# Optimization experiments

Measured on AMD Instinct MI355X. Metric: run time of the kernel, lower is better.

## Reference

```python
import jax, jax.numpy as jnp
import numpy as np

B, S, H, STATIC = 128, 128, 256, 2
BLOCKS = S // 2            # rotate_types = 2 for block_dim=2, allow_rot=True
DYN = 3 * BLOCKS           # dynamic channels: move / rotate_small / rotate_large


def setup_inputs() -> dict:
    key = jax.random.key(0)
    ks = jax.random.split(key, 16)
    p = lambda k, shape: (jax.random.normal(k, shape, jnp.float32) * 0.1)
    return {
        "static": jax.random.normal(ks[0], (B, STATIC + 1, S), jnp.float32),
        "dynamic": jnp.zeros((B, DYN, S), jnp.float32),
        "decoder_input": jax.random.normal(ks[1], (B, STATIC, 1), jnp.float32),
        # static/dynamic/decoder 1x1 conv encoders (weight [H, C_in], bias [H])
        "enc_s_W": p(ks[2], (H, STATIC)), "enc_s_b": p(ks[3], (H,)),
        "enc_d_W": p(ks[4], (H, DYN)),    "enc_d_b": p(ks[5], (H,)),
        "dec_W": p(ks[6], (H, STATIC)),   "dec_b": p(ks[7], (H,)),
        # single-layer GRU (torch layout: [3H, H] gates r,z,n)
        "gru_W_ih": p(ks[8], (3 * H, H)), "gru_W_hh": p(ks[9], (3 * H, H)),
        "gru_b_ih": p(ks[10], (3 * H,)),  "gru_b_hh": p(ks[11], (3 * H,)),
        # encoder attention and pointer heads: v [H], W [H, 3H]
        "attn_v": p(ks[12], (H,)), "attn_W": p(ks[13], (H, 3 * H)),
        "ptr_v": p(ks[14], (H,)),  "ptr_W": p(ks[15], (H, 3 * H)),
    }


def reference(static, dynamic, decoder_input,
              enc_s_W, enc_s_b, enc_d_W, enc_d_b, dec_W, dec_b,
              gru_W_ih, gru_W_hh, gru_b_ih, gru_b_hh,
              attn_v, attn_W, ptr_v, ptr_W):
    static_part = static[:, 1:, :]                                  # [B, STATIC, S]
    static_h = jnp.einsum('hi,bis->bhs', enc_s_W, static_part) + enc_s_b[None, :, None]
    dynamic_h = jnp.einsum('hi,bis->bhs', enc_d_W, dynamic) + enc_d_b[None, :, None]

    # initial mask from dynamic state (move + rotate feasibility)
    bn = dynamic.shape[1] // 3
    move = dynamic[:, :bn, :].sum(1)
    dyn_mask = dynamic[:, bn:2 * bn, :].sum(1) * dynamic[:, 2 * bn:3 * bn, :].sum(1) + move
    logmask = jnp.where(dyn_mask != 0, -jnp.inf, 0.0)               # log(current_mask), [B, S]

    hsz = gru_W_hh.shape[1]
    h0 = jnp.zeros((static.shape[0], hsz), static.dtype)            # GRU default zero state

    def gru_cell(x, h):
        gi = x @ gru_W_ih.T + gru_b_ih
        gh = h @ gru_W_hh.T + gru_b_hh
        ir, iz, inn = jnp.split(gi, 3, -1)
        hr, hz, hn = jnp.split(gh, 3, -1)
        r = jax.nn.sigmoid(ir + hr)
        z = jax.nn.sigmoid(iz + hz)
        n = jnp.tanh(inn + r * hn)
        return (1.0 - z) * n + z * h

    def step(carry, _):
        h_prev, dec_in = carry
        dec_h = jnp.einsum('hi,bi->bh', dec_W, dec_in[:, :, 0]) + dec_b   # decoder 1x1 conv
        h = gru_cell(dec_h, h_prev)                                       # rnn_out == new hidden
        rnn_b = jnp.broadcast_to(h[:, :, None], static_h.shape)
        hid = jnp.concatenate([static_h, dynamic_h, rnn_b], axis=1)       # [B, 3H, S]
        attn = jax.nn.softmax(
            jnp.einsum('h,bhs->bs', attn_v,
                       jnp.tanh(jnp.einsum('hk,bks->bhs', attn_W, hid))), axis=-1)
        context = jnp.einsum('bs,bhs->bh', attn, static_h)
        ctx_b = jnp.broadcast_to(context[:, :, None], static_h.shape)
        energy = jnp.concatenate([static_h, dynamic_h, ctx_b], axis=1)    # [B, 3H, S]
        logits = jnp.einsum('h,bhs->bs', ptr_v,
                            jnp.tanh(jnp.einsum('hk,bks->bhs', ptr_W, energy)))
        probs = jax.nn.softmax(logits + logmask, axis=-1)                 # [B, S]
        ptr = jnp.argmax(probs, axis=1)                                   # greedy (eval mode)
        logp = jnp.log(jnp.max(probs, axis=1))
        new_dec = jax.lax.stop_gradient(
            jnp.take_along_axis(static_part, ptr[:, None, None], axis=2))  # [B, STATIC, 1]
        return (h, new_dec), (ptr, logp)

    (_, _), (ptrs, logps) = jax.lax.scan(step, (h0, decoder_input), None,
                                         length=static_part.shape[2])
    tour_idx = ptrs.T    # [B, S]
    tour_logp = logps.T  # [B, S]
    return tour_idx, tour_logp
```

## Files before the change

kernel.cpp:

```cpp
#include <hip/hip_runtime.h>
#include <hip/hip_bf16.h>
#include <math.h>

#define BB   128
#define SS   128
#define HH   256
#define DYNN 192

#define OFF_FLAG  0
#define OFF_G     64
#define OFF_G0    (OFF_G + 1536)
#define OFF_M1A   (OFF_G0 + 768)
#define OFF_CA    (OFF_M1A + 512)
#define OFF_M1P   (OFF_CA + 256)
#define OFF_CP    (OFF_M1P + 512)
#define OFF_M3P   (OFF_CP + 256)
#define OFF_CP3   (OFF_M3P + 512)
#define OFF_LM    (OFF_CP3 + 256)
#define OFF_M2A   (OFF_LM + 16384)
#define OFF_M2P   (OFF_M2A + 49152)
#define OFF_BASEA (OFF_M2P + 49152)
#define OFF_BASEP (OFF_BASEA + 4194304)
#define OFF_END   (OFF_BASEP + 4194304)

__device__ __forceinline__ float tanh_fast(float x) {
    float e = __builtin_amdgcn_exp2f(x * 2.885390081777927f);
    return 1.0f - 2.0f * __builtin_amdgcn_rcpf(e + 1.0f);
}

__device__ __forceinline__ void ybar(int* cnt, bool arrive, int target) {
    if (arrive && (threadIdx.x & 63) == 0)
        __hip_atomic_fetch_add(cnt, 1, __ATOMIC_RELEASE, __HIP_MEMORY_SCOPE_WORKGROUP);
    while (__hip_atomic_load(cnt, __ATOMIC_ACQUIRE, __HIP_MEMORY_SCOPE_WORKGROUP) < target)
        __builtin_amdgcn_s_sleep(1);
}

__global__ void k1_logmask(const float* __restrict__ dyn, float* __restrict__ lm,
                           int* __restrict__ flag) {
    int g = blockIdx.x * 256 + threadIdx.x;
    if (g >= BB * SS) return;
    int b = g >> 7, s = g & 127;
    const float* p = dyn + (size_t)b * DYNN * SS + s;
    float mv = 0.f, m1 = 0.f, m2 = 0.f;
    bool nz = false;
    for (int i = 0; i < 64; ++i)        { float v = p[(size_t)i * SS]; mv += v; nz |= (v != 0.f); }
    for (int i = 64; i < 128; ++i)      { float v = p[(size_t)i * SS]; m1 += v; nz |= (v != 0.f); }
    for (int i = 128; i < 192; ++i)     { float v = p[(size_t)i * SS]; m2 += v; nz |= (v != 0.f); }
    float dm = m1 * m2 + mv;
    lm[g] = (dm != 0.f) ? -__builtin_inff() : 0.f;
    if (nz) atomicOr(flag, 1);
}

__global__ void k0a_folds(const float* __restrict__ Wih, const float* __restrict__ bih,
                          const float* __restrict__ dW,  const float* __restrict__ db,
                          const float* __restrict__ aW,  const float* __restrict__ pW,
                          const float* __restrict__ esW, const float* __restrict__ esb,
                          const float* __restrict__ edb, float* __restrict__ wsf) {
    int idx = blockIdx.x * 256 + threadIdx.x;
    float* G   = wsf + OFF_G;
    float* g0  = wsf + OFF_G0;
    float* M1a = wsf + OFF_M1A;
    float* ca  = wsf + OFF_CA;
    float* M1p = wsf + OFF_M1P;
    float* cp  = wsf + OFF_CP;
    float* M3p = wsf + OFF_M3P;
    float* cp3 = wsf + OFF_CP3;
    if (idx < 1536) {
        int r = idx >> 1, j = idx & 1;
        float a = 0.f;
        for (int k = 0; k < 256; ++k) a += Wih[r * 256 + k] * dW[k * 2 + j];
        G[idx] = a;
    } else if (idx < 2304) {
        int r = idx - 1536;
        float a = 0.f;
        for (int k = 0; k < 256; ++k) a += Wih[r * 256 + k] * db[k];
        g0[r] = a + bih[r];
    } else if (idx < 2816) {
        int t = idx - 2304; int h = t >> 1, j = t & 1;
        float a = 0.f;
        for (int k = 0; k < 256; ++k) a += aW[h * 768 + k] * esW[k * 2 + j];
        M1a[t] = a;
    } else if (idx < 3072) {
        int h = idx - 2816;
        float a = 0.f, b2 = 0.f;
        for (int k = 0; k < 256; ++k) a  += aW[h * 768 + k]       * esb[k];
        for (int k = 0; k < 256; ++k) b2 += aW[h * 768 + 256 + k] * edb[k];
        ca[h] = a + b2;
    } else if (idx < 3584) {
        int t = idx - 3072; int h = t >> 1, j = t & 1;
        float a = 0.f;
        for (int k = 0; k < 256; ++k) a += pW[h * 768 + k] * esW[k * 2 + j];
        M1p[t] = a;
    } else if (idx < 3840) {
        int h = idx - 3584;
        float a = 0.f, b2 = 0.f;
        for (int k = 0; k < 256; ++k) a  += pW[h * 768 + k]       * esb[k];
        for (int k = 0; k < 256; ++k) b2 += pW[h * 768 + 256 + k] * edb[k];
        cp[h] = a + b2;
    } else if (idx < 4352) {
        int t = idx - 3840; int h = t >> 1, j = t & 1;
        float a = 0.f;
        for (int k = 0; k < 256; ++k) a += pW[h * 768 + 512 + k] * esW[k * 2 + j];
        M3p[t] = a;
    } else if (idx < 4608) {
        int h = idx - 4352;
        float a = 0.f;
        for (int k = 0; k < 256; ++k) a += pW[h * 768 + 512 + k] * esb[k];
        cp3[h] = a;
    }
}

__global__ void k0b_m2(const float* __restrict__ aW, const float* __restrict__ pW,
                       const float* __restrict__ edW, float* __restrict__ wsf,
                       const int* __restrict__ flag) {
    if (*flag == 0) return;
    int idx = blockIdx.x * 256 + threadIdx.x;
    if (idx >= 2 * 49152) return;
    int which = idx / 49152;
    int t = idx % 49152;
    int h = t / DYNN, i = t % DYNN;
    const float* W = which ? pW : aW;
    float a = 0.f;
    for (int k = 0; k < 256; ++k) a += W[h * 768 + 256 + k] * edW[k * DYNN + i];
    wsf[(which ? OFF_M2P : OFF_M2A) + t] = a;
}

__global__ void k2_bases(const float* __restrict__ stat, const float* __restrict__ dyn,
                         float* __restrict__ wsf, const int* __restrict__ flag) {
    if (*flag == 0) return;
    __shared__ float col[DYNN];
    __shared__ float s01[2];
    const float* M1a = wsf + OFF_M1A; const float* ca  = wsf + OFF_CA;
    const float* M1p = wsf + OFF_M1P; const float* cp  = wsf + OFF_CP;
    const float* M2a = wsf + OFF_M2A; const float* M2p = wsf + OFF_M2P;
    float* basea = wsf + OFF_BASEA;   float* basep = wsf + OFF_BASEP;
    for (int pair = blockIdx.x; pair < BB * SS; pair += gridDim.x) {
        int b = pair >> 7, s = pair & 127;
        if (threadIdx.x < DYNN) col[threadIdx.x] = dyn[((size_t)b * DYNN + threadIdx.x) * SS + s];
        if (threadIdx.x == DYNN) {
            s01[0] = stat[((size_t)b * 3 + 1) * SS + s];
            s01[1] = stat[((size_t)b * 3 + 2) * SS + s];
        }
        __syncthreads();
        int h = threadIdx.x;
        float aa = fmaf(M1a[h * 2], s01[0], fmaf(M1a[h * 2 + 1], s01[1], ca[h]));
        float pp = fmaf(M1p[h * 2], s01[0], fmaf(M1p[h * 2 + 1], s01[1], cp[h]));
        for (int i = 0; i < DYNN; ++i) {
            aa = fmaf(M2a[h * DYNN + i], col[i], aa);
            pp = fmaf(M2p[h * DYNN + i], col[i], pp);
        }
        basea[((size_t)b * SS + s) * HH + h] = aa;
        basep[((size_t)b * SS + s) * HH + h] = pp;
        __syncthreads();
    }
}

__global__ __launch_bounds__(1024, 4) void k3_seq(
    const float* __restrict__ stat, const float* __restrict__ dec_inp,
    const float* __restrict__ Whh, const float* __restrict__ bhh_g,
    const float* __restrict__ aW, const float* __restrict__ av,
    const float* __restrict__ pv, const float* __restrict__ wsf,
    int allow_general, float* __restrict__ out) {
    const int b = blockIdx.x;
    const int tid = threadIdx.x;

    __shared__ float sh_gh[768], sh_hv[256], sh_t1[256], sh_a[128];
    __shared__ float sh_sp0[128], sh_sp1[128], sh_lm[128];
    __shared__ float sh_M1a[512], sh_M1p[512], sh_M3p[512];
    __shared__ float sh_ca[256], sh_cp[256], sh_cp3[256];
    __shared__ float sh_G[1536], sh_g0[768], sh_bhh[768];
    __shared__ float sh_va[256], sh_vp[256];
    __shared__ float sh_scal[4];
    __shared__ int ycnt;

    const float* G_   = wsf + OFF_G;   const float* g0_  = wsf + OFF_G0;
    const float* M1a_ = wsf + OFF_M1A; const float* ca_  = wsf + OFF_CA;
    const float* M1p_ = wsf + OFF_M1P; const float* cp_  = wsf + OFF_CP;
    const float* M3p_ = wsf + OFF_M3P; const float* cp3_ = wsf + OFF_CP3;
    const float* lm_  = wsf + OFF_LM;
    const float* basea = wsf + OFF_BASEA;
    const float* basep = wsf + OFF_BASEP;
    const int* flag = (const int*)wsf;

    for (int i = tid; i < 1536; i += 1024) sh_G[i] = G_[i];
    for (int i = tid; i < 768; i += 1024) {
        sh_g0[i] = g0_[i];
        float bv = bhh_g[i];
        sh_bhh[i] = bv;
        sh_gh[i] = bv;
    }
    for (int i = tid; i < 512; i += 1024) { sh_M1a[i] = M1a_[i]; sh_M1p[i] = M1p_[i]; sh_M3p[i] = M3p_[i]; }
    for (int i = tid; i < 256; i += 1024) {
        sh_ca[i] = ca_[i]; sh_cp[i] = cp_[i]; sh_cp3[i] = cp3_[i];
        sh_va[i] = av[i];  sh_vp[i] = pv[i];  sh_hv[i] = 0.f;
    }
    for (int i = tid; i < 128; i += 1024) {
        sh_sp0[i] = stat[((size_t)b * 3 + 1) * SS + i];
        sh_sp1[i] = stat[((size_t)b * 3 + 2) * SS + i];
        sh_lm[i]  = lm_[b * SS + i];
    }
    if (tid == 0) {
        sh_scal[0] = dec_inp[b * 2 + 0];
        sh_scal[1] = dec_inp[b * 2 + 1];
        ycnt = 0;
    }
    const bool dz = (!allow_general) || (*flag == 0);

    const int a3r = tid >> 2, a3q = tid & 3;
    float4 a3c[16];
    {
        const float4* src = (const float4*)(aW + (size_t)a3r * 768 + 512 + a3q * 64);
        #pragma unroll
        for (int i = 0; i < 16; ++i) a3c[i] = src[i];
    }
    __syncthreads();

    const int xg = tid >> 4, xj = tid & 15;

    for (int t = 0; t < SS; ++t) {
        if (tid < 256) {
            int k = tid;
            float d0 = sh_scal[0], d1 = sh_scal[1];
            float gr = fmaf(sh_G[k * 2],          d0, fmaf(sh_G[k * 2 + 1],          d1, sh_g0[k]));
            float gz = fmaf(sh_G[(k + 256) * 2],  d0, fmaf(sh_G[(k + 256) * 2 + 1],  d1, sh_g0[k + 256]));
            float gn = fmaf(sh_G[(k + 512) * 2],  d0, fmaf(sh_G[(k + 512) * 2 + 1],  d1, sh_g0[k + 512]));
            float r = 1.f / (1.f + expf(-(gr + sh_gh[k])));
            float z = 1.f / (1.f + expf(-(gz + sh_gh[k + 256])));
            float n = tanhf(gn + r * sh_gh[k + 512]);
            sh_hv[k] = (1.f - z) * n + z * sh_hv[k];
        }
        __syncthreads();

        {
            float acc = 0.f;
            const float4* h4 = (const float4*)sh_hv;
            #pragma unroll
            for (int i = 0; i < 16; ++i) {
                float4 w = a3c[i];
                float4 x = h4[a3q * 16 + i];
                acc = fmaf(w.x, x.x, fmaf(w.y, x.y, fmaf(w.z, x.z, fmaf(w.w, x.w, acc))));
            }
            acc += __shfl_xor(acc, 1, 4);
            acc += __shfl_xor(acc, 2, 4);
            if (a3q == 0) sh_t1[a3r] = acc + (dz ? sh_ca[a3r] : 0.f);
        }
        __syncthreads();

        if (tid < 512) {
            if (t < SS - 1) {
                float4 hx0 = ((const float4*)sh_hv)[xj];
                float4 hx1 = ((const float4*)sh_hv)[xj + 16];
                float4 hx2 = ((const float4*)sh_hv)[xj + 32];
                float4 hx3 = ((const float4*)sh_hv)[xj + 48];
                #pragma unroll 2
                for (int k = 0; k < 24; ++k) {
                    int r = xg + 32 * k;
                    const float4* Wr = (const float4*)(Whh + (size_t)r * 256);
                    float4 w0 = Wr[xj];
                    float4 w1 = Wr[xj + 16];
                    float4 w2 = Wr[xj + 32];
                    float4 w3 = Wr[xj + 48];
                    float acc = 0.f;
                    acc = fmaf(w0.x, hx0.x, fmaf(w0.y, hx0.y, fmaf(w0.z, hx0.z, fmaf(w0.w, hx0.w, acc))));
                    acc = fmaf(w1.x, hx1.x, fmaf(w1.y, hx1.y, fmaf(w1.z, hx1.z, fmaf(w1.w, hx1.w, acc))));
                    acc = fmaf(w2.x, hx2.x, fmaf(w2.y, hx2.y, fmaf(w2.z, hx2.z, fmaf(w2.w, hx2.w, acc))));
                    acc = fmaf(w3.x, hx3.x, fmaf(w3.y, hx3.y, fmaf(w3.z, hx3.z, fmaf(w3.w, hx3.w, acc))));
                    acc += __shfl_xor(acc, 1, 16); acc += __shfl_xor(acc, 2, 16);
                    acc += __shfl_xor(acc, 4, 16); acc += __shfl_xor(acc, 8, 16);
                    if (xj == 0) sh_gh[r] = acc + sh_bhh[r];
                }
            }
        } else {
            const int yt = tid - 512;
            const int ybase = t * 17;

            {
                int s = yt >> 2, g = yt & 3;
                float acc = 0.f;
                if (dz) {
                    float s0 = sh_sp0[s], s1 = sh_sp1[s];
                    #pragma unroll 8
                    for (int i = g; i < 256; i += 4) {
                        float arg = fmaf(sh_M1a[i * 2], s0, fmaf(sh_M1a[i * 2 + 1], s1, sh_t1[i]));
                        acc = fmaf(sh_va[i], tanh_fast(arg), acc);
                    }
                } else {
                    const float* bb = basea + ((size_t)b * SS + s) * HH;
                    #pragma unroll 8
                    for (int i = g; i < 256; i += 4)
                        acc = fmaf(sh_va[i], tanh_fast(bb[i] + sh_t1[i]), acc);
                }
                acc += __shfl_xor(acc, 1, 4); acc += __shfl_xor(acc, 2, 4);
                if (g == 0) sh_a[s] = acc;
            }
            ybar(&ycnt, true, ybase + 8);

            if (yt < 64) {
                int lane = yt;
                float v0 = sh_a[lane], v1 = sh_a[lane + 64];
                float m = fmaxf(v0, v1);
                for (int msk = 1; msk < 64; msk <<= 1) m = fmaxf(m, __shfl_xor(m, msk, 64));
                float e0 = expf(v0 - m), e1 = expf(v1 - m);
                float S = e0 + e1;
                float c0 = e0 * sh_sp0[lane] + e1 * sh_sp0[lane + 64];
                float c1 = e0 * sh_sp1[lane] + e1 * sh_sp1[lane + 64];
                for (int msk = 1; msk < 64; msk <<= 1) {
                    S  += __shfl_xor(S,  msk, 64);
                    c0 += __shfl_xor(c0, msk, 64);
                    c1 += __shfl_xor(c1, msk, 64);
                }
                float C0 = c0 / S, C1 = c1 / S;
                #pragma unroll
                for (int q = 0; q < 4; ++q) {
                    int k2 = lane + 64 * q;
                    float v = fmaf(sh_M3p[k2 * 2], C0, fmaf(sh_M3p[k2 * 2 + 1], C1, sh_cp3[k2]));
                    sh_t1[k2] = v + (dz ? sh_cp[k2] : 0.f);
                }
                ybar(&ycnt, true, ybase + 9);
            } else {
                ybar(&ycnt, false, ybase + 9);
            }

            {
                int s = yt >> 2, g = yt & 3;
                float acc = 0.f;
                if (dz) {
                    float s0 = sh_sp0[s], s1 = sh_sp1[s];
                    #pragma unroll 8
                    for (int i = g; i < 256; i += 4) {
                        float arg = fmaf(sh_M1p[i * 2], s0, fmaf(sh_M1p[i * 2 + 1], s1, sh_t1[i]));
                        acc = fmaf(sh_vp[i], tanh_fast(arg), acc);
                    }
                } else {
                    const float* bb = basep + ((size_t)b * SS + s) * HH;
                    #pragma unroll 8
                    for (int i = g; i < 256; i += 4)
                        acc = fmaf(sh_vp[i], tanh_fast(bb[i] + sh_t1[i]), acc);
                }
                acc += __shfl_xor(acc, 1, 4); acc += __shfl_xor(acc, 2, 4);
                if (g == 0) sh_a[s] = acc;
            }
            ybar(&ycnt, true, ybase + 17);

            if (yt < 64) {
                int lane = yt;
                float l0 = sh_a[lane] + sh_lm[lane];
                float l1 = sh_a[lane + 64] + sh_lm[lane + 64];
                float v; int idx;
                if (l0 >= l1) { v = l0; idx = lane; } else { v = l1; idx = lane + 64; }
                for (int msk = 1; msk < 64; msk <<= 1) {
                    float ov = __shfl_xor(v, msk, 64);
                    int   oi = __shfl_xor(idx, msk, 64);
                    if (ov > v || (ov == v && oi < idx)) { v = ov; idx = oi; }
                }
                float S = expf(l0 - v) + expf(l1 - v);
                for (int msk = 1; msk < 64; msk <<= 1) S += __shfl_xor(S, msk, 64);
                if (lane == 0) {
                    out[b * SS + t] = (float)idx;
                    out[BB * SS + b * SS + t] = -logf(S);
                    sh_scal[0] = sh_sp0[idx];
                    sh_scal[1] = sh_sp1[idx];
                }
            }
        }
        __syncthreads();
    }
}

extern "C" void kernel_launch(void* const* d_in, const int* in_sizes, int n_in,
                              void* d_out, int out_size, void* d_ws, size_t ws_size,
                              hipStream_t stream) {
    const float* stat  = (const float*)d_in[0];
    const float* dyn   = (const float*)d_in[1];
    const float* decin = (const float*)d_in[2];
    const float* esW   = (const float*)d_in[3];
    const float* esb   = (const float*)d_in[4];
    const float* edW   = (const float*)d_in[5];
    const float* edb   = (const float*)d_in[6];
    const float* dW    = (const float*)d_in[7];
    const float* db    = (const float*)d_in[8];
    const float* Wih   = (const float*)d_in[9];
    const float* Whh   = (const float*)d_in[10];
    const float* bih   = (const float*)d_in[11];
    const float* bhh   = (const float*)d_in[12];
    const float* av    = (const float*)d_in[13];
    const float* aW    = (const float*)d_in[14];
    const float* pv    = (const float*)d_in[15];
    const float* pW    = (const float*)d_in[16];
    float* wsf = (float*)d_ws;
    int* flag  = (int*)d_ws;
    float* out = (float*)d_out;

    int allow_general = (ws_size >= (size_t)OFF_END * 4) ? 1 : 0;

    hipMemsetAsync(d_ws, 0, 64 * 4, stream);
    hipLaunchKernelGGL(k1_logmask, dim3(64), dim3(256), 0, stream, dyn, wsf + OFF_LM, flag);
    hipLaunchKernelGGL(k0a_folds, dim3(18), dim3(256), 0, stream,
                       Wih, bih, dW, db, aW, pW, esW, esb, edb, wsf);
    if (allow_general) {
        hipLaunchKernelGGL(k0b_m2, dim3(384), dim3(256), 0, stream, aW, pW, edW, wsf, flag);
        hipLaunchKernelGGL(k2_bases, dim3(256), dim3(256), 0, stream, stat, dyn, wsf, flag);
    }
    hipLaunchKernelGGL(k3_seq, dim3(128), dim3(1024), 0, stream,
                       stat, decin, Whh, bhh, aW, av, pv, wsf, allow_general, out);
}
```

Before: 1.830 ms.

## Move attention hidden projection to consumer warps and cache part of W_hh in LDS

The attention W·h projection used to be computed by all 1024 threads from register-cached weights, behind a full block barrier. It now runs only in the upper 512 threads (the attention/pointer half), reading weights from global memory, and is synchronized with the named counter barrier. This removes one __syncthreads per step and lets the GRU W_hh matvec overlap with it. The first 96 rows of W_hh are staged in a ~96KB LDS buffer to cut global reads, and the occupancy hint in launch_bounds is relaxed, at the cost of large shared memory use and more barrier stages in the consumer half.

```diff
diff --git a/kernel.cpp b/kernel.cpp
--- a/kernel.cpp
+++ b/kernel.cpp
@@ -6,6 +6,7 @@
 #define SS   128
 #define HH   256
 #define DYNN 192
+#define LC   96
 
 #define OFF_FLAG  0
 #define OFF_G     64
@@ -155,7 +156,7 @@
     }
 }
 
-__global__ __launch_bounds__(1024, 4) void k3_seq(
+__global__ __launch_bounds__(1024) void k3_seq(
     const float* __restrict__ stat, const float* __restrict__ dec_inp,
     const float* __restrict__ Whh, const float* __restrict__ bhh_g,
     const float* __restrict__ aW, const float* __restrict__ av,
@@ -164,6 +165,7 @@
     const int b = blockIdx.x;
     const int tid = threadIdx.x;
 
+    __shared__ float sh_whh[LC][256];
     __shared__ float sh_gh[768], sh_hv[256], sh_t1[256], sh_a[128];
     __shared__ float sh_sp0[128], sh_sp1[128], sh_lm[128];
     __shared__ float sh_M1a[512], sh_M1p[512], sh_M3p[512];
@@ -182,6 +184,11 @@
     const float* basep = wsf + OFF_BASEP;
     const int* flag = (const int*)wsf;
 
+    {
+        float4* dst = (float4*)&sh_whh[0][0];
+        const float4* src = (const float4*)Whh;
+        for (int i = tid; i < LC * 64; i += 1024) dst[i] = src[i];
+    }
     for (int i = tid; i < 1536; i += 1024) sh_G[i] = G_[i];
     for (int i = tid; i < 768; i += 1024) {
         sh_g0[i] = g0_[i];
@@ -205,17 +212,7 @@
         ycnt = 0;
     }
     const bool dz = (!allow_general) || (*flag == 0);
-
-    const int a3r = tid >> 2, a3q = tid & 3;
-    float4 a3c[16];
-    {
-        const float4* src = (const float4*)(aW + (size_t)a3r * 768 + 512 + a3q * 64);
-        #pragma unroll
-        for (int i = 0; i < 16; ++i) a3c[i] = src[i];
-    }
     __syncthreads();
-
-    const int xg = tid >> 4, xj = tid & 15;
 
     for (int t = 0; t < SS; ++t) {
         if (tid < 256) {
@@ -231,29 +228,32 @@
         }
         __syncthreads();
 
-        {
-            float acc = 0.f;
-            const float4* h4 = (const float4*)sh_hv;
-            #pragma unroll
-            for (int i = 0; i < 16; ++i) {
-                float4 w = a3c[i];
-                float4 x = h4[a3q * 16 + i];
-                acc = fmaf(w.x, x.x, fmaf(w.y, x.y, fmaf(w.z, x.z, fmaf(w.w, x.w, acc))));
-            }
-            acc += __shfl_xor(acc, 1, 4);
-            acc += __shfl_xor(acc, 2, 4);
-            if (a3q == 0) sh_t1[a3r] = acc + (dz ? sh_ca[a3r] : 0.f);
-        }
-        __syncthreads();
-
         if (tid < 512) {
-            if (t < SS - 1) {
+            if (t + 1 < SS) {
+                const int xg = tid >> 4, xj = tid & 15;
                 float4 hx0 = ((const float4*)sh_hv)[xj];
                 float4 hx1 = ((const float4*)sh_hv)[xj + 16];
                 float4 hx2 = ((const float4*)sh_hv)[xj + 32];
                 float4 hx3 = ((const float4*)sh_hv)[xj + 48];
+                #pragma unroll
+                for (int k = 0; k < 3; ++k) {
+                    int r = xg + 32 * k;
+                    const float4* Wr = (const float4*)&sh_whh[r][0];
+                    float4 w0 = Wr[xj];
+                    float4 w1 = Wr[xj + 16];
+                    float4 w2 = Wr[xj + 32];
+                    float4 w3 = Wr[xj + 48];
+                    float acc = 0.f;
+                    acc = fmaf(w0.x, hx0.x, fmaf(w0.y, hx0.y, fmaf(w0.z, hx0.z, fmaf(w0.w, hx0.w, acc))));
+                    acc = fmaf(w1.x, hx1.x, fmaf(w1.y, hx1.y, fmaf(w1.z, hx1.z, fmaf(w1.w, hx1.w, acc))));
+                    acc = fmaf(w2.x, hx2.x, fmaf(w2.y, hx2.y, fmaf(w2.z, hx2.z, fmaf(w2.w, hx2.w, acc))));
+                    acc = fmaf(w3.x, hx3.x, fmaf(w3.y, hx3.y, fmaf(w3.z, hx3.z, fmaf(w3.w, hx3.w, acc))));
+                    acc += __shfl_xor(acc, 1, 16); acc += __shfl_xor(acc, 2, 16);
+                    acc += __shfl_xor(acc, 4, 16); acc += __shfl_xor(acc, 8, 16);
+                    if (xj == 0) sh_gh[r] = acc + sh_bhh[r];
+                }
                 #pragma unroll 2
-                for (int k = 0; k < 24; ++k) {
+                for (int k = 3; k < 24; ++k) {
                     int r = xg + 32 * k;
                     const float4* Wr = (const float4*)(Whh + (size_t)r * 256);
                     float4 w0 = Wr[xj];
@@ -272,7 +272,33 @@
             }
         } else {
             const int yt = tid - 512;
-            const int ybase = t * 17;
+            const int ybase = t * 25;
+
+            {
+                const int yq = yt >> 4, yj = yt & 15;
+                float4 hx0 = ((const float4*)sh_hv)[yj];
+                float4 hx1 = ((const float4*)sh_hv)[yj + 16];
+                float4 hx2 = ((const float4*)sh_hv)[yj + 32];
+                float4 hx3 = ((const float4*)sh_hv)[yj + 48];
+                #pragma unroll 2
+                for (int k = 0; k < 8; ++k) {
+                    int r = yq + 32 * k;
+                    const float4* Wr = (const float4*)(aW + (size_t)r * 768 + 512);
+                    float4 w0 = Wr[yj];
+                    float4 w1 = Wr[yj + 16];
+                    float4 w2 = Wr[yj + 32];
+                    float4 w3 = Wr[yj + 48];
+                    float acc = 0.f;
+                    acc = fmaf(w0.x, hx0.x, fmaf(w0.y, hx0.y, fmaf(w0.z, hx0.z, fmaf(w0.w, hx0.w, acc))));
+                    acc = fmaf(w1.x, hx1.x, fmaf(w1.y, hx1.y, fmaf(w1.z, hx1.z, fmaf(w1.w, hx1.w, acc))));
+                    acc = fmaf(w2.x, hx2.x, fmaf(w2.y, hx2.y, fmaf(w2.z, hx2.z, fmaf(w2.w, hx2.w, acc))));
+                    acc = fmaf(w3.x, hx3.x, fmaf(w3.y, hx3.y, fmaf(w3.z, hx3.z, fmaf(w3.w, hx3.w, acc))));
+                    acc += __shfl_xor(acc, 1, 16); acc += __shfl_xor(acc, 2, 16);
+                    acc += __shfl_xor(acc, 4, 16); acc += __shfl_xor(acc, 8, 16);
+                    if (yj == 0) sh_t1[r] = acc + (dz ? sh_ca[r] : 0.f);
+                }
+            }
+            ybar(&ycnt, true, ybase + 8);
 
             {
                 int s = yt >> 2, g = yt & 3;
@@ -293,7 +319,7 @@
                 acc += __shfl_xor(acc, 1, 4); acc += __shfl_xor(acc, 2, 4);
                 if (g == 0) sh_a[s] = acc;
             }
-            ybar(&ycnt, true, ybase + 8);
+            ybar(&ycnt, true, ybase + 16);
 
             if (yt < 64) {
                 int lane = yt;
@@ -316,9 +342,9 @@
                     float v = fmaf(sh_M3p[k2 * 2], C0, fmaf(sh_M3p[k2 * 2 + 1], C1, sh_cp3[k2]));
                     sh_t1[k2] = v + (dz ? sh_cp[k2] : 0.f);
                 }
-                ybar(&ycnt, true, ybase + 9);
+                ybar(&ycnt, true, ybase + 17);
             } else {
-                ybar(&ycnt, false, ybase + 9);
+                ybar(&ycnt, false, ybase + 17);
             }
 
             {
@@ -340,7 +366,7 @@
                 acc += __shfl_xor(acc, 1, 4); acc += __shfl_xor(acc, 2, 4);
                 if (g == 0) sh_a[s] = acc;
             }
-            ybar(&ycnt, true, ybase + 17);
+            ybar(&ycnt, true, ybase + 25);
 
             if (yt < 64) {
                 int lane = yt;
@@ -393,7 +419,7 @@
 
     int allow_general = (ws_size >= (size_t)OFF_END * 4) ? 1 : 0;
 
-    hipMemsetAsync(d_ws, 0, 64 * 4, stream);
+    hipMemsetAsync(d_ws, 0, 256, stream);
     hipLaunchKernelGGL(k1_logmask, dim3(64), dim3(256), 0, stream, dyn, wsf + OFF_LM, flag);
     hipLaunchKernelGGL(k0a_folds, dim3(18), dim3(256), 0, stream,
                        Wih, bih, dW, db, aW, pW, esW, esb, edb, wsf);
```

Result: slower. 2.230 ms (+21.8%).
